# Kernel tuning notes

Measured on AMD Instinct MI355X. Metric: run time of the kernel, lower is better.

## Reference

```python
import jax, jax.numpy as jnp
import numpy as np


def setup_inputs() -> dict:
    key = jax.random.key(0)
    k1, k2 = jax.random.split(key)
    B, N = 2, 8192
    pred = jax.random.normal(k1, (B, N, 3), dtype=jnp.float32)
    gt = jax.random.normal(k2, (B, N, 3), dtype=jnp.float32)
    return {"pred": pred, "gt": gt}


def reference(pred, gt):
    # dist[b, i, j] = ||pred[b, j] - gt[b, i]||_2, computed via the
    # squared-norm expansion to avoid materializing a [B,N,N,3] diff tensor.
    p_sq = jnp.sum(pred * pred, axis=-1)  # [B, N]
    g_sq = jnp.sum(gt * gt, axis=-1)      # [B, N]
    # inner[b, i, j] = gt[b, i] . pred[b, j]
    inner = jnp.einsum("bid,bjd->bij", gt, pred)  # [B, N, N]
    sq_dist = g_sq[:, :, None] + p_sq[:, None, :] - 2.0 * inner
    dist = jnp.sqrt(jnp.maximum(sq_dist, 0.0))    # [B, N, N]
    dist1 = jnp.min(dist, axis=2)  # per-gt nearest pred distance, [B, N]
    dist2 = jnp.min(dist, axis=1)  # per-pred nearest gt distance, [B, N]
    chamfer = (dist1.mean(axis=1) + dist2.mean(axis=1)).mean()
    return chamfer
```

## Files before the change

kernel.cpp:

```cpp
#include <hip/hip_runtime.h>
#include <math.h>

#define NPTS  8192
#define BATCH 2
#define GY    64
#define CJ    (NPTS / GY)
#define IPT   8
#define TPB   256
#define NSLOT (2 * BATCH * NPTS)
#define GX    (NSLOT / (TPB * IPT))

typedef float v2f __attribute__((ext_vector_type(2)));
typedef float v4f __attribute__((ext_vector_type(4)));

__global__ __launch_bounds__(TPB) void chamfer_pairs(
    const float* __restrict__ pred, const float* __restrict__ gt,
    unsigned int* __restrict__ mins)
{
    __shared__ v4f xs4[CJ / 4], ys4[CJ / 4], zs4[CJ / 4], qs4[CJ / 4];

    const int base  = blockIdx.x * (TPB * IPT);
    const int dir   = base >> 14;
    const int b     = (base >> 13) & 1;
    const int ibase = base & (NPTS - 1);

    const float* pts  = (dir == 0 ? gt : pred) + (size_t)b * NPTS * 3;
    const float* cand = (dir == 0 ? pred : gt) + (size_t)b * NPTS * 3;

    const int j0 = blockIdx.y * CJ;
    if (threadIdx.x < CJ) {
        int jj = threadIdx.x;
        float x = cand[(size_t)(j0 + jj) * 3 + 0];
        float y = cand[(size_t)(j0 + jj) * 3 + 1];
        float z = cand[(size_t)(j0 + jj) * 3 + 2];
        ((float*)xs4)[jj] = x; ((float*)ys4)[jj] = y; ((float*)zs4)[jj] = z;
        ((float*)qs4)[jj] = 0.5f * (x * x + y * y + z * z);
    }

    float px[IPT], py[IPT], pz[IPT], m[IPT];
#pragma unroll
    for (int k = 0; k < IPT; ++k) {
        int i = ibase + threadIdx.x + k * TPB;
        px[k] = pts[(size_t)i * 3 + 0];
        py[k] = pts[(size_t)i * 3 + 1];
        pz[k] = pts[(size_t)i * 3 + 2];
        m[k]  = 3.0e38f;
    }
    __syncthreads();

#pragma unroll 4
    for (int j = 0; j < CJ / 4; ++j) {
        v4f cx = xs4[j], cy = ys4[j], cz = zs4[j], cq = qs4[j];
        v2f cxa = cx.xy, cxb = cx.zw, cya = cy.xy, cyb = cy.zw;
        v2f cza = cz.xy, czb = cz.zw, cqa = cq.xy, cqb = cq.zw;
#pragma unroll
        for (int k = 0; k < IPT; ++k) {
            v2f ta = cqa - cxa * px[k];
            ta = ta - cya * py[k];
            ta = ta - cza * pz[k];
            v2f tb = cqb - cxb * px[k];
            tb = tb - cyb * py[k];
            tb = tb - czb * pz[k];
            m[k] = fminf(fminf(m[k], ta.x), ta.y);
            m[k] = fminf(fminf(m[k], tb.x), tb.y);
        }
    }

#pragma unroll
    for (int k = 0; k < IPT; ++k) {
        float gsq = fmaf(px[k], px[k], fmaf(py[k], py[k], pz[k] * pz[k]));
        float d2  = fmaxf(fmaf(2.0f, m[k], gsq), 0.0f);
        atomicMin(&mins[base + k * TPB + threadIdx.x], __float_as_uint(d2));
    }
}

__global__ __launch_bounds__(1024) void chamfer_reduce(
    const unsigned int* __restrict__ mins, float* __restrict__ out)
{
    float s = 0.f;
#pragma unroll
    for (int r = 0; r < NSLOT / 1024; ++r)
        s += sqrtf(__uint_as_float(mins[r * 1024 + threadIdx.x]));

    for (int off = 32; off > 0; off >>= 1)
        s += __shfl_down(s, off, 64);

    __shared__ float ws[16];
    const int wave = threadIdx.x >> 6, lane = threadIdx.x & 63;
    if (lane == 0) ws[wave] = s;
    __syncthreads();
    if (threadIdx.x == 0) {
        float t = 0.f;
#pragma unroll
        for (int w = 0; w < 16; ++w) t += ws[w];
        out[0] = t * (1.0f / (float)(BATCH * NPTS));
    }
}

extern "C" void kernel_launch(void* const* d_in, const int* in_sizes, int n_in,
                              void* d_out, int out_size, void* d_ws, size_t ws_size,
                              hipStream_t stream) {
    const float* pred = (const float*)d_in[0];
    const float* gt   = (const float*)d_in[1];
    unsigned int* mins = (unsigned int*)d_ws;

    dim3 grid(GX, GY);
    chamfer_pairs<<<grid, TPB, 0, stream>>>(pred, gt, mins);
    chamfer_reduce<<<1, 1024, 0, stream>>>(mins, (float*)d_out);
}
```

Baseline: 78.22 us.

## Pre-pack candidates into SoA global arrays and read them as uniform loads

Adds a pack kernel that writes candidate x, y, z and half squared norm into structure-of-arrays buffers in the workspace. The pair kernel now reads candidates straight from global memory with wave-uniform addresses, likely scalar loads, so it no longer needs LDS staging or a block barrier. The cost is one extra launch and extra workspace. The inner loop is also reduced to processing 2 candidates per step. The mins buffer is not initialised in the code shown, so it presumably relies on an external reset, and its workspace offset has moved.

```diff
diff --git a/kernel.cpp b/kernel.cpp
--- a/kernel.cpp
+++ b/kernel.cpp
@@ -11,31 +11,40 @@
 #define GX    (NSLOT / (TPB * IPT))
 
 typedef float v2f __attribute__((ext_vector_type(2)));
-typedef float v4f __attribute__((ext_vector_type(4)));
+
+__global__ __launch_bounds__(256) void chamfer_pack(
+    const float* __restrict__ pred, const float* __restrict__ gt,
+    float* __restrict__ xs, float* __restrict__ ys,
+    float* __restrict__ zs, float* __restrict__ qs)
+{
+    const int cs  = blockIdx.x * 256 + threadIdx.x;
+    const int dir = cs >> 14;
+    const int b   = (cs >> 13) & 1;
+    const int j   = cs & (NPTS - 1);
+    const float* c = (dir == 0 ? pred : gt) + ((size_t)b * NPTS + j) * 3;
+    float x = c[0], y = c[1], z = c[2];
+    xs[cs] = x; ys[cs] = y; zs[cs] = z;
+    qs[cs] = 0.5f * (x * x + y * y + z * z);
+}
 
 __global__ __launch_bounds__(TPB) void chamfer_pairs(
     const float* __restrict__ pred, const float* __restrict__ gt,
+    const float* __restrict__ xs, const float* __restrict__ ys,
+    const float* __restrict__ zs, const float* __restrict__ qs,
     unsigned int* __restrict__ mins)
 {
-    __shared__ v4f xs4[CJ / 4], ys4[CJ / 4], zs4[CJ / 4], qs4[CJ / 4];
-
     const int base  = blockIdx.x * (TPB * IPT);
     const int dir   = base >> 14;
     const int b     = (base >> 13) & 1;
     const int ibase = base & (NPTS - 1);
 
-    const float* pts  = (dir == 0 ? gt : pred) + (size_t)b * NPTS * 3;
-    const float* cand = (dir == 0 ? pred : gt) + (size_t)b * NPTS * 3;
+    const float* pts = (dir == 0 ? gt : pred) + (size_t)b * NPTS * 3;
 
-    const int j0 = blockIdx.y * CJ;
-    if (threadIdx.x < CJ) {
-        int jj = threadIdx.x;
-        float x = cand[(size_t)(j0 + jj) * 3 + 0];
-        float y = cand[(size_t)(j0 + jj) * 3 + 1];
-        float z = cand[(size_t)(j0 + jj) * 3 + 2];
-        ((float*)xs4)[jj] = x; ((float*)ys4)[jj] = y; ((float*)zs4)[jj] = z;
-        ((float*)qs4)[jj] = 0.5f * (x * x + y * y + z * z);
-    }
+    const int co = (base & 24576) + blockIdx.y * CJ;
+    const float* cxp = xs + co;
+    const float* cyp = ys + co;
+    const float* czp = zs + co;
+    const float* cqp = qs + co;
 
     float px[IPT], py[IPT], pz[IPT], m[IPT];
 #pragma unroll
@@ -46,23 +55,19 @@
         pz[k] = pts[(size_t)i * 3 + 2];
         m[k]  = 3.0e38f;
     }
-    __syncthreads();
 
 #pragma unroll 4
-    for (int j = 0; j < CJ / 4; ++j) {
-        v4f cx = xs4[j], cy = ys4[j], cz = zs4[j], cq = qs4[j];
-        v2f cxa = cx.xy, cxb = cx.zw, cya = cy.xy, cyb = cy.zw;
-        v2f cza = cz.xy, czb = cz.zw, cqa = cq.xy, cqb = cq.zw;
+    for (int j = 0; j < CJ; j += 2) {
+        v2f cx = {cxp[j], cxp[j + 1]};
+        v2f cy = {cyp[j], cyp[j + 1]};
+        v2f cz = {czp[j], czp[j + 1]};
+        v2f cq = {cqp[j], cqp[j + 1]};
 #pragma unroll
         for (int k = 0; k < IPT; ++k) {
-            v2f ta = cqa - cxa * px[k];
-            ta = ta - cya * py[k];
-            ta = ta - cza * pz[k];
-            v2f tb = cqb - cxb * px[k];
-            tb = tb - cyb * py[k];
-            tb = tb - czb * pz[k];
-            m[k] = fminf(fminf(m[k], ta.x), ta.y);
-            m[k] = fminf(fminf(m[k], tb.x), tb.y);
+            v2f t = cq - cx * px[k];
+            t = t - cy * py[k];
+            t = t - cz * pz[k];
+            m[k] = fminf(fminf(m[k], t.x), t.y);
         }
     }
 
@@ -102,9 +107,14 @@
                               hipStream_t stream) {
     const float* pred = (const float*)d_in[0];
     const float* gt   = (const float*)d_in[1];
-    unsigned int* mins = (unsigned int*)d_ws;
+    float* xs = (float*)d_ws;
+    float* ys = xs + NSLOT;
+    float* zs = ys + NSLOT;
+    float* qs = zs + NSLOT;
+    unsigned int* mins = (unsigned int*)(qs + NSLOT);
 
+    chamfer_pack<<<NSLOT / 256, 256, 0, stream>>>(pred, gt, xs, ys, zs, qs);
     dim3 grid(GX, GY);
-    chamfer_pairs<<<grid, TPB, 0, stream>>>(pred, gt, mins);
+    chamfer_pairs<<<grid, TPB, 0, stream>>>(pred, gt, xs, ys, zs, qs, mins);
     chamfer_reduce<<<1, 1024, 0, stream>>>(mins, (float*)d_out);
 }
```

Measured after the change: 83.40 us. 1.07x slower.
